# Kernel tuning notes

Hardware: AMD Instinct MI355X
Metric: run time of the kernel (lower is better)

Reference implementation:

```python
import jax, jax.numpy as jnp
import numpy as np

H = 256
B, S = 8, 2048
WIN = 16


def setup_inputs() -> dict:
    key = jax.random.key(0)
    k1, k2, k3, k4, k5 = jax.random.split(key, 5)
    bound = 1.0 / np.sqrt(H)  # torch nn.RNN init range
    x = jax.random.normal(k1, (B, S, H), dtype=jnp.float32)
    W_ih = jax.random.uniform(k2, (H, H), jnp.float32, -bound, bound)
    W_hh = jax.random.uniform(k3, (H, H), jnp.float32, -bound, bound)
    b_ih = jax.random.uniform(k4, (H,), jnp.float32, -bound, bound)
    b_hh = jax.random.uniform(k5, (H,), jnp.float32, -bound, bound)
    return {"x": x, "W_ih": W_ih, "W_hh": W_hh, "b_ih": b_ih, "b_hh": b_hh, "window": WIN}


def reference(x, W_ih, W_hh, b_ih, b_hh, window):
    # Original: get_K builds [B, S, window, H] overlapping windows (left-padded
    # with window-1 zeros), runs an RNN over each length-`window` sequence with
    # h0 = 0, and keeps the last hidden state -> [B, S, H].
    # Equivalent streaming form: at step k of the window, every position t
    # consumes xpad[:, t + k]; so slice a shifted view of the padded input and
    # update all B*S hidden states at once (never materializing the windows).
    b, s, h = x.shape
    xpad = jnp.pad(x, ((0, 0), (window - 1, 0), (0, 0)))  # [B, S+W-1, H]

    def step(hid, k):
        xk = jax.lax.dynamic_slice(xpad, (0, k, 0), (b, s, h))  # [B, S, H]
        hid = jnp.tanh(xk @ W_ih.T + b_ih + hid @ W_hh.T + b_hh)
        return hid, None

    h0 = jnp.zeros((b, s, h), dtype=x.dtype)
    h_last, _ = jax.lax.scan(step, h0, jnp.arange(window))
    return h_last  # [B, S, H]
```

## Files before the change

### kernel.cpp

```cpp
#include <hip/hip_runtime.h>

#define HDIM 256
#define SEQ 2048
#define TPOS 64

typedef _Float16 half8_t __attribute__((ext_vector_type(8)));
typedef float floatx16 __attribute__((ext_vector_type(16)));

#define U_PITCH 1024
#define H_PITCH 512
#define U_ROWS 79
#define H0_OFF (U_ROWS * U_PITCH)
#define H1_OFF (H0_OFF + 64 * H_PITCH)
#define LDS_BYTES (H0_OFF + 2 * 64 * H_PITCH)

static __device__ __forceinline__ float exp2f_fast(float x) {
  float r; asm("v_exp_f32 %0, %1" : "=v"(r) : "v"(x)); return r;
}
static __device__ __forceinline__ float rcpf_fast(float x) {
  float r; asm("v_rcp_f32 %0, %1" : "=v"(r) : "v"(x)); return r;
}
static __device__ __forceinline__ float tanhf_fast(float x) {
  float e = exp2f_fast(x * 2.8853900817779268f);
  return 1.0f - 2.0f * rcpf_fast(e + 1.0f);
}
static __device__ __forceinline__ unsigned pkh(float a, float b) {
  return __builtin_bit_cast(unsigned, __builtin_amdgcn_cvt_pkrtz(a, b));
}

__global__ __launch_bounds__(512, 2) void winrnn_kernel(
    const float* __restrict__ x, const float* __restrict__ W_ih,
    const float* __restrict__ W_hh, const float* __restrict__ b_ih,
    const float* __restrict__ b_hh, float* __restrict__ out) {
  extern __shared__ char smem[];
  const int tid = threadIdx.x;
  const int w = tid >> 6;
  const int lane = tid & 63;
  const int l31 = lane & 31;
  const int hi = lane >> 5;

  const int wg = blockIdx.x;
  const int batch = wg >> 5;
  const int t0 = (wg & 31) * TPOS;
  const float* xb = x + (size_t)batch * SEQ * HDIM;

  const int jgroup = w >> 1;
  const int pt = w & 1;
  const int jbase = jgroup * 64;
  const int p_loc = pt * 32 + l31;

  {
    char* xl = smem + H0_OFF;
#pragma unroll
    for (int it = 0; it < 12; ++it) {
      int idx = tid + it * 512;
      int row = idx >> 6;
      int c4 = idx & 63;
      int xi = t0 - 15 + row;
      float4 v = make_float4(0.f, 0.f, 0.f, 0.f);
      if (row < U_ROWS && xi >= 0)
        v = *reinterpret_cast<const float4*>(xb + (size_t)xi * HDIM + c4 * 4);
      uint2 u;
      u.x = pkh(v.x, v.y);
      u.y = pkh(v.z, v.w);
      *reinterpret_cast<uint2*>(xl + row * H_PITCH + ((c4 * 8) ^ ((row & 31) << 4))) = u;
    }
  }

  half8_t Wf[2][16];
#pragma unroll
  for (int jt = 0; jt < 2; ++jt)
#pragma unroll
    for (int kt = 0; kt < 16; ++kt) {
      const float* wp = W_ih + (size_t)(jbase + jt * 32 + l31) * HDIM + kt * 16 + hi * 8;
      float4 a = *reinterpret_cast<const float4*>(wp);
      float4 b = *reinterpret_cast<const float4*>(wp + 4);
      uint4 uu;
      uu.x = pkh(a.x, a.y); uu.y = pkh(a.z, a.w);
      uu.z = pkh(b.x, b.y); uu.w = pkh(b.z, b.w);
      Wf[jt][kt] = __builtin_bit_cast(half8_t, uu);
    }

  float4 biasf[2][4];
#pragma unroll
  for (int jt = 0; jt < 2; ++jt)
#pragma unroll
    for (int g = 0; g < 4; ++g) {
      int j0 = jbase + jt * 32 + g * 8 + hi * 4;
      float4 bi = *reinterpret_cast<const float4*>(b_ih + j0);
      float4 bh = *reinterpret_cast<const float4*>(b_hh + j0);
      biasf[jt][g] = make_float4(bi.x + bh.x, bi.y + bh.y, bi.z + bh.z, bi.w + bh.w);
    }

  __syncthreads();

  {
    const char* xl = smem + H0_OFF;
    char* Ul = smem;
    int nps = (pt == 0) ? 2 : 1;
    for (int s = 0; s < nps; ++s) {
      int prow = (pt + s * 2) * 32 + l31;
      floatx16 acc0, acc1;
#pragma unroll
      for (int g = 0; g < 4; ++g) {
        acc0[4*g+0] = biasf[0][g].x; acc0[4*g+1] = biasf[0][g].y;
        acc0[4*g+2] = biasf[0][g].z; acc0[4*g+3] = biasf[0][g].w;
        acc1[4*g+0] = biasf[1][g].x; acc1[4*g+1] = biasf[1][g].y;
        acc1[4*g+2] = biasf[1][g].z; acc1[4*g+3] = biasf[1][g].w;
      }
#pragma unroll
      for (int kt = 0; kt < 16; ++kt) {
        half8_t xB = *reinterpret_cast<const half8_t*>(
            xl + prow * H_PITCH + ((kt * 32 + hi * 16) ^ ((prow & 31) << 4)));
        acc0 = __builtin_amdgcn_mfma_f32_32x32x16_f16(Wf[0][kt], xB, acc0, 0, 0, 0);
        acc1 = __builtin_amdgcn_mfma_f32_32x32x16_f16(Wf[1][kt], xB, acc1, 0, 0, 0);
      }
      if (prow < U_ROWS) {
#pragma unroll
        for (int jt = 0; jt < 2; ++jt)
#pragma unroll
          for (int g = 0; g < 4; ++g) {
            int j0 = jbase + jt * 32 + g * 8 + hi * 4;
            float4 st;
            const floatx16& ac = jt ? acc1 : acc0;
            st.x = ac[4*g+0]; st.y = ac[4*g+1]; st.z = ac[4*g+2]; st.w = ac[4*g+3];
            *reinterpret_cast<float4*>(Ul + prow * U_PITCH + ((j0 * 4) ^ ((prow & 31) << 4))) = st;
          }
      }
    }
  }

#pragma unroll
  for (int jt = 0; jt < 2; ++jt)
#pragma unroll
    for (int kt = 0; kt < 16; ++kt) {
      const float* wp = W_hh + (size_t)(jbase + jt * 32 + l31) * HDIM + kt * 16 + hi * 8;
      float4 a = *reinterpret_cast<const float4*>(wp);
      float4 b = *reinterpret_cast<const float4*>(wp + 4);
      uint4 uu;
      uu.x = pkh(a.x, a.y); uu.y = pkh(a.z, a.w);
      uu.z = pkh(b.x, b.y); uu.w = pkh(b.z, b.w);
      Wf[jt][kt] = __builtin_bit_cast(half8_t, uu);
    }

  __syncthreads();

  const char* Ul = smem;
  char* hb0 = smem + H0_OFF;
  char* hb1 = smem + H1_OFF;
  float* outp = out + ((size_t)batch * SEQ + t0 + p_loc) * HDIM;
  const int hswz = (p_loc & 31) << 4;

  for (int k = 0; k < 16; ++k) {
    floatx16 acc0, acc1;
    int urow = p_loc + k;
    int uswz = (urow & 31) << 4;
#pragma unroll
    for (int g = 0; g < 4; ++g) {
      int j00 = (jbase + g * 8 + hi * 4) * 4;
      float4 u0 = *reinterpret_cast<const float4*>(Ul + urow * U_PITCH + (j00 ^ uswz));
      float4 u1 = *reinterpret_cast<const float4*>(Ul + urow * U_PITCH + ((j00 + 128) ^ uswz));
      acc0[4*g+0] = u0.x; acc0[4*g+1] = u0.y; acc0[4*g+2] = u0.z; acc0[4*g+3] = u0.w;
      acc1[4*g+0] = u1.x; acc1[4*g+1] = u1.y; acc1[4*g+2] = u1.z; acc1[4*g+3] = u1.w;
    }
    if (k > 0) {
      const char* hr = ((k & 1) ? hb0 : hb1);
#pragma unroll
      for (int kt = 0; kt < 16; ++kt) {
        half8_t hB = *reinterpret_cast<const half8_t*>(
            hr + p_loc * H_PITCH + ((kt * 32 + hi * 16) ^ hswz));
        acc0 = __builtin_amdgcn_mfma_f32_32x32x16_f16(Wf[0][kt], hB, acc0, 0, 0, 0);
        acc1 = __builtin_amdgcn_mfma_f32_32x32x16_f16(Wf[1][kt], hB, acc1, 0, 0, 0);
      }
    }
    if (k < 15) {
      char* hw = ((k & 1) ? hb1 : hb0);
#pragma unroll
      for (int jt = 0; jt < 2; ++jt) {
        const floatx16& ac = jt ? acc1 : acc0;
#pragma unroll
        for (int g = 0; g < 4; ++g) {
          float ta = tanhf_fast(ac[4*g+0]);
          float tb = tanhf_fast(ac[4*g+1]);
          float tc = tanhf_fast(ac[4*g+2]);
          float td = tanhf_fast(ac[4*g+3]);
          uint2 u; u.x = pkh(ta, tb); u.y = pkh(tc, td);
          int jb = (jbase + jt * 32 + g * 8 + hi * 4) * 2;
          *reinterpret_cast<uint2*>(hw + p_loc * H_PITCH + (jb ^ hswz)) = u;
        }
      }
    } else {
#pragma unroll
      for (int jt = 0; jt < 2; ++jt) {
        const floatx16& ac = jt ? acc1 : acc0;
#pragma unroll
        for (int g = 0; g < 4; ++g) {
          float4 st;
          st.x = tanhf_fast(ac[4*g+0]); st.y = tanhf_fast(ac[4*g+1]);
          st.z = tanhf_fast(ac[4*g+2]); st.w = tanhf_fast(ac[4*g+3]);
          *reinterpret_cast<float4*>(outp + jbase + jt * 32 + g * 8 + hi * 4) = st;
        }
      }
    }
    __syncthreads();
  }
}

extern "C" void kernel_launch(void* const* d_in, const int* in_sizes, int n_in,
                              void* d_out, int out_size, void* d_ws, size_t ws_size,
                              hipStream_t stream) {
  const float* x    = (const float*)d_in[0];
  const float* W_ih = (const float*)d_in[1];
  const float* W_hh = (const float*)d_in[2];
  const float* b_ih = (const float*)d_in[3];
  const float* b_hh = (const float*)d_in[4];
  float* out = (float*)d_out;
  static_assert(LDS_BYTES <= 160 * 1024, "LDS budget");
  hipFuncSetAttribute(reinterpret_cast<const void*>(winrnn_kernel),
                      hipFuncAttributeMaxDynamicSharedMemorySize, LDS_BYTES);
  winrnn_kernel<<<dim3(256), dim3(512), LDS_BYTES, stream>>>(x, W_ih, W_hh, b_ih, b_hh, out);
}
```

Before: 74.40 us.

## Halve positions per workgroup and stage final outputs through LDS

```diff
diff --git a/kernel.cpp b/kernel.cpp
--- a/kernel.cpp
+++ b/kernel.cpp
@@ -2,17 +2,17 @@
 
 #define HDIM 256
 #define SEQ 2048
-#define TPOS 64
+#define TPOS 32
 
 typedef _Float16 half8_t __attribute__((ext_vector_type(8)));
 typedef float floatx16 __attribute__((ext_vector_type(16)));
 
 #define U_PITCH 1024
 #define H_PITCH 512
-#define U_ROWS 79
+#define U_ROWS 47
 #define H0_OFF (U_ROWS * U_PITCH)
-#define H1_OFF (H0_OFF + 64 * H_PITCH)
-#define LDS_BYTES (H0_OFF + 2 * 64 * H_PITCH)
+#define H1_OFF (H0_OFF + 32 * H_PITCH)
+#define LDS_BYTES (H0_OFF + 2 * 32 * H_PITCH)
 
 static __device__ __forceinline__ float exp2f_fast(float x) {
   float r; asm("v_exp_f32 %0, %1" : "=v"(r) : "v"(x)); return r;
@@ -28,7 +28,7 @@
   return __builtin_bit_cast(unsigned, __builtin_amdgcn_cvt_pkrtz(a, b));
 }
 
-__global__ __launch_bounds__(512, 2) void winrnn_kernel(
+__global__ __launch_bounds__(256, 2) void winrnn_kernel(
     const float* __restrict__ x, const float* __restrict__ W_ih,
     const float* __restrict__ W_hh, const float* __restrict__ b_ih,
     const float* __restrict__ b_hh, float* __restrict__ out) {
@@ -40,20 +40,19 @@
   const int hi = lane >> 5;
 
   const int wg = blockIdx.x;
-  const int batch = wg >> 5;
-  const int t0 = (wg & 31) * TPOS;
+  const int batch = wg >> 6;
+  const int t0 = (wg & 63) * TPOS;
   const float* xb = x + (size_t)batch * SEQ * HDIM;
 
-  const int jgroup = w >> 1;
-  const int pt = w & 1;
-  const int jbase = jgroup * 64;
-  const int p_loc = pt * 32 + l31;
+  const int jbase = w * 64;
+  const int p_loc = l31;
+  const int hswz = l31 << 4;
 
   {
     char* xl = smem + H0_OFF;
 #pragma unroll
-    for (int it = 0; it < 12; ++it) {
-      int idx = tid + it * 512;
+    for (int it = 0; it < 16; ++it) {
+      int idx = tid + it * 256;
       int row = idx >> 6;
       int c4 = idx & 63;
       int xi = t0 - 15 + row;
@@ -97,9 +96,9 @@
   {
     const char* xl = smem + H0_OFF;
     char* Ul = smem;
-    int nps = (pt == 0) ? 2 : 1;
-    for (int s = 0; s < nps; ++s) {
-      int prow = (pt + s * 2) * 32 + l31;
+#pragma unroll
+    for (int s = 0; s < 2; ++s) {
+      int prow = s * 32 + l31;
       floatx16 acc0, acc1;
 #pragma unroll
       for (int g = 0; g < 4; ++g) {
@@ -148,11 +147,9 @@
   const char* Ul = smem;
   char* hb0 = smem + H0_OFF;
   char* hb1 = smem + H1_OFF;
-  float* outp = out + ((size_t)batch * SEQ + t0 + p_loc) * HDIM;
-  const int hswz = (p_loc & 31) << 4;
-
+
+  floatx16 acc0, acc1;
   for (int k = 0; k < 16; ++k) {
-    floatx16 acc0, acc1;
     int urow = p_loc + k;
     int uswz = (urow & 31) << 4;
 #pragma unroll
@@ -189,20 +186,40 @@
           *reinterpret_cast<uint2*>(hw + p_loc * H_PITCH + (jb ^ hswz)) = u;
         }
       }
-    } else {
-#pragma unroll
-      for (int jt = 0; jt < 2; ++jt) {
-        const floatx16& ac = jt ? acc1 : acc0;
-#pragma unroll
-        for (int g = 0; g < 4; ++g) {
-          float4 st;
-          st.x = tanhf_fast(ac[4*g+0]); st.y = tanhf_fast(ac[4*g+1]);
-          st.z = tanhf_fast(ac[4*g+2]); st.w = tanhf_fast(ac[4*g+3]);
-          *reinterpret_cast<float4*>(outp + jbase + jt * 32 + g * 8 + hi * 4) = st;
-        }
-      }
-    }
-    __syncthreads();
+      __syncthreads();
+    }
+  }
+
+  __syncthreads();
+  {
+    char* ol = smem + H0_OFF;
+    const int oswz = (p_loc & 31) << 4;
+#pragma unroll
+    for (int jt = 0; jt < 2; ++jt) {
+      const floatx16& ac = jt ? acc1 : acc0;
+#pragma unroll
+      for (int g = 0; g < 4; ++g) {
+        float4 st;
+        st.x = tanhf_fast(ac[4*g+0]); st.y = tanhf_fast(ac[4*g+1]);
+        st.z = tanhf_fast(ac[4*g+2]); st.w = tanhf_fast(ac[4*g+3]);
+        int jb = (jbase + jt * 32 + g * 8 + hi * 4) * 4;
+        *reinterpret_cast<float4*>(ol + p_loc * 1024 + (jb ^ oswz)) = st;
+      }
+    }
+  }
+  __syncthreads();
+  {
+    const char* ol = smem + H0_OFF;
+    float* ob = out + ((size_t)batch * SEQ + t0) * HDIM;
+#pragma unroll
+    for (int it = 0; it < 8; ++it) {
+      int idx = tid + it * 256;
+      int row = idx >> 6;
+      int c = idx & 63;
+      float4 v = *reinterpret_cast<const float4*>(
+          ol + row * 1024 + ((c * 16) ^ ((row & 31) << 4)));
+      *reinterpret_cast<float4*>(ob + (size_t)row * HDIM + c * 4) = v;
+    }
   }
 }
 
@@ -215,8 +232,8 @@
   const float* b_ih = (const float*)d_in[3];
   const float* b_hh = (const float*)d_in[4];
   float* out = (float*)d_out;
-  static_assert(LDS_BYTES <= 160 * 1024, "LDS budget");
+  static_assert(2 * LDS_BYTES <= 160 * 1024, "need 2 WGs/CU");
   hipFuncSetAttribute(reinterpret_cast<const void*>(winrnn_kernel),
                       hipFuncAttributeMaxDynamicSharedMemorySize, LDS_BYTES);
-  winrnn_kernel<<<dim3(256), dim3(512), LDS_BYTES, stream>>>(x, W_ih, W_hh, b_ih, b_hh, out);
-}
+  winrnn_kernel<<<dim3(512), dim3(256), LDS_BYTES, stream>>>(x, W_ih, W_hh, b_ih, b_hh, out);
+}
```

Result: no change. 73.37 us (-1.4%).
